# Optimization experiments

Hardware: AMD Instinct MI355X
Metric: run time of the kernel (lower is better)

## Reference

```python
import jax, jax.numpy as jnp
import numpy as np

NH = 16  # attention heads
TOPK = 50

def _rms(x, w):
    return x * jax.lax.rsqrt(jnp.mean(x * x, axis=-1, keepdims=True) + 1e-6) * w

def _rope(x, pos):
    # x: [1, T, NH, HD], pos: [T]
    half = x.shape[-1] // 2
    inv = 1.0 / (10000.0 ** (jnp.arange(half, dtype=jnp.float32) / half))
    ang = pos.astype(jnp.float32)[:, None] * inv[None, :]          # [T, half]
    cos = jnp.cos(ang)[None, :, None, :]
    sin = jnp.sin(ang)[None, :, None, :]
    x1, x2 = x[..., :half], x[..., half:]
    return jnp.concatenate([x1 * cos - x2 * sin, x2 * cos + x1 * sin], axis=-1)


def setup_inputs() -> dict:
    key = jax.random.key(0)
    ks = jax.random.split(key, 12)
    G, V, D, NL, FF = 15, 2048, 1024, 2, 4096
    s = 0.02
    return {
        'talker_hidden': jax.random.normal(ks[0], (1, 1, D), jnp.float32),
        'code_0_embed': jax.random.normal(ks[1], (1, 1, D), jnp.float32),
        'temperature': jnp.ones((1,), jnp.float32),
        'sample_uniforms': jax.random.uniform(ks[2], (G,), jnp.float32),
        'stacked_heads': jax.random.normal(ks[3], (G, V, D), jnp.float32) * s,
        'stacked_embeds': jax.random.normal(ks[4], (G, V, D), jnp.float32) * s,
        'ln1': jnp.ones((NL, D), jnp.float32),
        'ln2': jnp.ones((NL, D), jnp.float32),
        'ln_f': jnp.ones((D,), jnp.float32),
        'wq': jax.random.normal(ks[5], (NL, D, D), jnp.float32) * s,
        'wk': jax.random.normal(ks[6], (NL, D, D), jnp.float32) * s,
        'wv': jax.random.normal(ks[7], (NL, D, D), jnp.float32) * s,
        'wo': jax.random.normal(ks[8], (NL, D, D), jnp.float32) * s,
        'w1': jax.random.normal(ks[9], (NL, D, FF), jnp.float32) * s,
        'w2': jax.random.normal(ks[10], (NL, FF, D), jnp.float32) * s,
    }


def reference(talker_hidden, code_0_embed, temperature, sample_uniforms,
              stacked_heads, stacked_embeds, ln1, ln2, ln_f,
              wq, wk, wv, wo, w1, w2):
    NL = wq.shape[0]
    D = wq.shape[1]
    HD = D // NH
    G = stacked_heads.shape[0]

    def transformer_step(h, qpos, caches):
        # h: [1, T, D]; qpos: [T] absolute positions; caches: list of (k,v) or None
        new_caches = []
        for l in range(NL):
            T = h.shape[1]
            x = _rms(h, ln1[l])
            q = (x @ wq[l]).reshape(1, T, NH, HD)
            k = (x @ wk[l]).reshape(1, T, NH, HD)
            v = (x @ wv[l]).reshape(1, T, NH, HD)
            q = _rope(q, qpos)
            k = _rope(k, qpos)
            if caches is None:
                k_all, v_all = k, v
            else:
                k_all = jnp.concatenate([caches[l][0], k], axis=1)
                v_all = jnp.concatenate([caches[l][1], v], axis=1)
            new_caches.append((k_all, v_all))
            S = k_all.shape[1]
            scores = jnp.einsum('bthd,bshd->bhts', q, k_all) / jnp.sqrt(jnp.float32(HD))
            mask = jnp.arange(S)[None, :] <= qpos[:, None]      # [T, S] causal
            scores = jnp.where(mask[None, None], scores, jnp.float32(-1e30))
            attn = jax.nn.softmax(scores, axis=-1)
            out = jnp.einsum('bhts,bshd->bthd', attn, v_all).reshape(1, T, D)
            h = h + out @ wo[l]
            h = h + jax.nn.gelu((_rms(h, ln2[l])) @ w1[l]) @ w2[l]
        return _rms(h, ln_f), new_caches

    cp_input = jnp.concatenate([talker_hidden, code_0_embed], axis=1)  # [1, 2, D]
    h_seq, caches = transformer_step(cp_input, jnp.arange(2), None)
    hidden = h_seq[:, -1:, :]                                           # [1, 1, D]

    safe_temp = jnp.maximum(temperature.reshape(()), 1e-5)
    embed_sum = code_0_embed.reshape(-1)
    codes = []
    for g in range(G):
        logits = stacked_heads[g] @ hidden.reshape(-1)                  # [V]
        topv, topi = jax.lax.top_k(logits, TOPK)
        probs = jax.nn.softmax(topv / safe_temp)
        cdf = jnp.cumsum(probs)
        u = jnp.clip(sample_uniforms[g], 1e-6, 1.0 - 1e-6)
        choice = jnp.argmax((cdf >= u).astype(jnp.int32))
        code = topi[choice]
        codes.append(code.astype(jnp.int64))
        emb = stacked_embeds[g][code]                                   # [D]
        embed_sum = embed_sum + emb
        if g + 1 < G:
            h_seq, caches = transformer_step(emb[None, None, :],
                                             jnp.array([g + 2]), caches)
            hidden = h_seq[:, -1:, :]
    return jnp.stack(codes), embed_sum
```

## Files before the change

### kernel.cpp

```cpp
#include <hip/hip_runtime.h>
#include <math.h>

#define D      1024
#define NHEADS 16
#define HDIM   64
#define NL     2
#define FF     4096
#define NGRP   15
#define VOC    2048
#define TOPK   50
#define MAXS   16
#define NB     256
#define SLOT   16

struct Params {
    const float* talker; const float* code0; const float* temp; const float* unis;
    const float* heads;  const float* embeds;
    const float* ln1; const float* ln2; const float* lnf;
    const float* wq; const float* wk; const float* wv; const float* wo;
    const float* w1; const float* w2;
    float* out; float* ws;
};

__device__ __forceinline__ float cload(const float* p) {
    return __hip_atomic_load(p, __ATOMIC_RELAXED, __HIP_MEMORY_SCOPE_AGENT);
}
__device__ __forceinline__ void cstore(float* p, float v) {
    __hip_atomic_store(p, v, __ATOMIC_RELAXED, __HIP_MEMORY_SCOPE_AGENT);
}

__device__ __forceinline__ float wave_reduce_sum(float v) {
#pragma unroll
    for (int m = 32; m >= 1; m >>= 1) v += __shfl_xor(v, m, 64);
    return v;
}

__device__ __forceinline__ float geluf(float y) {
    return 0.5f * y * (1.f + tanhf(0.7978845608028654f * (y + 0.044715f * y * y * y)));
}

__device__ __forceinline__ void gsync(unsigned* arrive, unsigned* release, unsigned ep) {
    __syncthreads();
    const int bid = blockIdx.x, tid = threadIdx.x;
    if (tid == 0) {
        asm volatile("s_waitcnt vmcnt(0) lgkmcnt(0)" ::: "memory");
        __hip_atomic_store(&arrive[bid * SLOT], ep, __ATOMIC_RELAXED, __HIP_MEMORY_SCOPE_AGENT);
    }
    if (bid == 0) {
        while (__hip_atomic_load(&arrive[tid * SLOT], __ATOMIC_RELAXED,
                                 __HIP_MEMORY_SCOPE_AGENT) < ep)
            __builtin_amdgcn_s_sleep(4);
        __syncthreads();
        __hip_atomic_store(&release[tid * SLOT], ep, __ATOMIC_RELAXED, __HIP_MEMORY_SCOPE_AGENT);
    } else if (tid == 0) {
        while (__hip_atomic_load(&release[bid * SLOT], __ATOMIC_RELAXED,
                                 __HIP_MEMORY_SCOPE_AGENT) < ep)
            __builtin_amdgcn_s_sleep(4);
    }
    asm volatile("" ::: "memory");
    __syncthreads();
}

__device__ __forceinline__ void load_rms(const float* __restrict__ src,
                                         const float* __restrict__ w,
                                         float* xn, float* red) {
    int tid = threadIdx.x;
    float ss = 0.f;
    for (int i = tid; i < D; i += 256) { float v = cload(src + i); xn[i] = v; ss += v * v; }
    red[tid] = ss;
    __syncthreads();
    for (int s = 128; s > 0; s >>= 1) {
        if (tid < s) red[tid] += red[tid + s];
        __syncthreads();
    }
    float inv = rsqrtf(red[0] / (float)D + 1e-6f);
    for (int i = tid; i < D; i += 256) xn[i] = xn[i] * inv * w[i];
    __syncthreads();
}

__global__ __launch_bounds__(256) void k_pre(const float* __restrict__ th,
                                             const float* __restrict__ c0,
                                             float* __restrict__ h,
                                             float* __restrict__ out,
                                             float* __restrict__ qkv,
                                             unsigned* __restrict__ slots) {
    int i = blockIdx.x * 256 + threadIdx.x;
    if (i < 1024) {
        h[i] = th[i];
        h[D + i] = c0[i];
        out[NGRP + i] = c0[i];
    }
    for (int j = i; j < 2 * 3 * D; j += 2048) qkv[j] = 0.f;
    for (int j = i; j < 2 * NB * SLOT; j += 2048) slots[j] = 0u;
}

__global__ __launch_bounds__(256) void k_all(Params p) {
    __shared__ float xn[D];
    __shared__ float red[256];
    __shared__ float4 part[4][64];
    __shared__ float s_topv[TOPK];
    __shared__ int   s_topi[TOPK];
    __shared__ int   s_code;

    float* ws   = p.ws;
    float* h    = ws;
    float* qkvb = ws + 2048;
    float* ao   = ws + 8192;
    float* kc   = ws + 10240;
    float* vc   = ws + 43008;
    float* ub   = ws + 75776;
    float* lg   = ws + 83968;
    unsigned* arrive  = (unsigned*)(ws + 86016);
    unsigned* release = arrive + NB * SLOT;

    const int bid = blockIdx.x;
    const int tid = threadIdx.x;
    unsigned ep = 0;

    auto GS = [&]() { gsync(arrive, release, ++ep); };

    auto step = [&](int T, int basePos) {
        for (int l = 0; l < NL; ++l) {
            if (bid < 96 * T) {
                int x = bid % 12, y = (bid / 12) % 8, t = bid / 96;
                int m = x >> 2, ob = x & 3;
                load_rms(h + t * D, p.ln1 + l * D, xn, red);
                const float* W = ((m == 0) ? p.wq : (m == 1) ? p.wk : p.wv) + (long)l * D * D;
                int w = tid >> 6, lane = tid & 63;
                int obase = ob * 256;
                int kbase = (y * 4 + w) * 32;
                const float* Wp = W + (long)kbase * D + obase + lane * 4;
                float4 acc = {0.f, 0.f, 0.f, 0.f};
#pragma unroll 4
                for (int i = 0; i < 32; ++i) {
                    float xv = xn[kbase + i];
                    float4 wv4 = *(const float4*)(Wp + (long)i * D);
                    acc.x += xv * wv4.x; acc.y += xv * wv4.y;
                    acc.z += xv * wv4.z; acc.w += xv * wv4.w;
                }
                part[w][lane] = acc;
                __syncthreads();
                const float* pp = (const float*)part;
                float s = pp[tid] + pp[256 + tid] + pp[512 + tid] + pp[768 + tid];
                atomicAdd(&qkvb[t * 3 * D + m * D + obase + tid], s);
            }
            GS();

            {
                for (int i = bid * 256 + tid; i < T * FF; i += NB * 256) cstore(&ub[i], 0.f);
                int wid = bid * 4 + (tid >> 6);
                if (wid < T * NHEADS) {
                    int t = wid / NHEADS, hd = wid % NHEADS, d = tid & 63;
                    float* kcl = kc + (long)l * MAXS * D;
                    float* vcl = vc + (long)l * MAXS * D;
                    int pos = basePos + t;
                    int i = d & 31;
                    float inv = __expf(-(float)i * (9.210340371976184f / 32.0f));
                    float ang = (float)pos * inv;
                    float cs = cosf(ang), sn = sinf(ang);

                    float q = cload(&qkvb[t * 3 * D + hd * HDIM + d]);
                    float qp = __shfl_xor(q, 32, 64);
                    float qr = (d < 32) ? (q * cs - qp * sn) : (q * cs + qp * sn);

                    float k0 = cload(&qkvb[t * 3 * D + D + hd * HDIM + d]);
                    float kp = __shfl_xor(k0, 32, 64);
                    float kr = (d < 32) ? (k0 * cs - kp * sn) : (k0 * cs + kp * sn);

                    float v0 = cload(&qkvb[t * 3 * D + 2 * D + hd * HDIM + d]);
                    cstore(&kcl[pos * D + hd * HDIM + d], kr);
                    cstore(&vcl[pos * D + hd * HDIM + d], v0);

                    float sc[MAXS];
#pragma unroll
                    for (int s = 0; s < MAXS; ++s) {
                        if (s > pos) break;
                        float kv;
                        if (s < basePos) {
                            kv = cload(&kcl[s * D + hd * HDIM + d]);
                        } else if (s == pos) {
                            kv = kr;
                        } else {
                            float kk = cload(&qkvb[(s - basePos) * 3 * D + D + hd * HDIM + d]);
                            float kkp = __shfl_xor(kk, 32, 64);
                            float a2 = (float)s * inv;
                            float c2 = cosf(a2), s2 = sinf(a2);
                            kv = (d < 32) ? (kk * c2 - kkp * s2) : (kk * c2 + kkp * s2);
                        }
                        float dt = wave_reduce_sum(qr * kv);
                        sc[s] = dt * 0.125f;
                    }
                    float mx = -1e30f;
#pragma unroll
                    for (int s = 0; s < MAXS; ++s) { if (s > pos) break; mx = fmaxf(mx, sc[s]); }
                    float lsum = 0.f;
#pragma unroll
                    for (int s = 0; s < MAXS; ++s) { if (s > pos) break; sc[s] = expf(sc[s] - mx); lsum += sc[s]; }
                    float o = 0.f;
#pragma unroll
                    for (int s = 0; s < MAXS; ++s) {
                        if (s > pos) break;
                        float vv = (s < basePos) ? cload(&vcl[s * D + hd * HDIM + d])
                                                 : cload(&qkvb[(s - basePos) * 3 * D + 2 * D + hd * HDIM + d]);
                        o += sc[s] * vv;
                    }
                    cstore(&ao[t * D + hd * HDIM + d], o / lsum);
                }
            }
            GS();

            {
                for (int i = bid * 256 + tid; i < T * 3 * D; i += NB * 256) cstore(&qkvb[i], 0.f);
                if (bid < 64 * T) {
                    int x = bid % 4, y = (bid / 4) % 16, t = bid / 64;
                    const float* W = p.wo + (long)l * D * D;
                    for (int i = tid; i < D; i += 256) xn[i] = cload(&ao[t * D + i]);
                    __syncthreads();
                    int w = tid >> 6, lane = tid & 63;
                    int obase = x * 256;
                    int kbase = (y * 4 + w) * 16;
                    const float* Wp = W + (long)kbase * D + obase + lane * 4;
                    float4 acc = {0.f, 0.f, 0.f, 0.f};
#pragma unroll 4
                    for (int i = 0; i < 16; ++i) {
                        float xv = xn[kbase + i];
                        float4 wv4 = *(const float4*)(Wp + (long)i * D);
                        acc.x += xv * wv4.x; acc.y += xv * wv4.y;
                        acc.z += xv * wv4.z; acc.w += xv * wv4.w;
                    }
                    part[w][lane] = acc;
                    __syncthreads();
                    const float* pp = (const float*)part;
                    float s = pp[tid] + pp[256 + tid] + pp[512 + tid] + pp[768 + tid];
                    atomicAdd(&h[t * D + obase + tid], s);
                }
            }
            GS();

            if (bid < 128 * T) {
                int x = bid % 16, y = (bid / 16) % 8, t = bid / 128;
                load_rms(h + t * D, p.ln2 + l * D, xn, red);
                const float* W = p.w1 + (long)l * D * FF;
                int w = tid >> 6, lane = tid & 63;
                int obase = x * 256;
                int kbase = (y * 4 + w) * 32;
                const float* Wp = W + (long)kbase * FF + obase + lane * 4;
                float4 acc = {0.f, 0.f, 0.f, 0.f};
#pragma unroll 4
                for (int i = 0; i < 32; ++i) {
                    float xv = xn[kbase + i];
                    float4 wv4 = *(const float4*)(Wp + (long)i * FF);
                    acc.x += xv * wv4.x; acc.y += xv * wv4.y;
                    acc.z += xv * wv4.z; acc.w += xv * wv4.w;
                }
                part[w][lane] = acc;
                __syncthreads();
                const float* pp = (const float*)part;
                float s = pp[tid] + pp[256 + tid] + pp[512 + tid] + pp[768 + tid];
                atomicAdd(&ub[t * FF + obase + tid], s);
            }
            GS();

            if (bid < 128 * T) {
                int x = bid % 4, y = (bid / 4) % 32, t = bid / 128;
                int kblk = y * 128;
                if (tid < 128) red[tid] = geluf(cload(&ub[t * FF + kblk + tid]));
                __syncthreads();
                const float* W = p.w2 + (long)l * FF * D;
                int w = tid >> 6, lane = tid & 63;
                int obase = x * 256;
                int kloc = w * 32;
                const float* Wp = W + (long)(kblk + kloc) * D + obase + lane * 4;
                float4 acc = {0.f, 0.f, 0.f, 0.f};
#pragma unroll 4
                for (int i = 0; i < 32; ++i) {
                    float xv = red[kloc + i];
                    float4 wv4 = *(const float4*)(Wp + (long)i * D);
                    acc.x += xv * wv4.x; acc.y += xv * wv4.y;
                    acc.z += xv * wv4.z; acc.w += xv * wv4.w;
                }
                part[w][lane] = acc;
                __syncthreads();
                const float* pp = (const float*)part;
                float s = pp[tid] + pp[256 + tid] + pp[512 + tid] + pp[768 + tid];
                atomicAdd(&h[t * D + obase + tid], s);
            }
            GS();
        }
    };

    step(2, 0);

    for (int g = 0; g < NGRP; ++g) {
        {
            const float* hid = h + ((g == 0) ? D : 0);
            if (bid < 128) {
                load_rms(hid, p.lnf, xn, red);
                int lane = tid & 63, w = tid >> 6;
                int rbase = bid * 16 + w * 4;
                const float* Hd = p.heads + (long)g * VOC * D;
#pragma unroll
                for (int r = 0; r < 4; ++r) {
                    const float* row = Hd + (long)(rbase + r) * D;
                    float acc = 0.f;
#pragma unroll
                    for (int it = 0; it < 4; ++it) {
                        int idx = it * 256 + lane * 4;
                        float4 a = *(const float4*)(row + idx);
                        acc += a.x * xn[idx] + a.y * xn[idx + 1]
                             + a.z * xn[idx + 2] + a.w * xn[idx + 3];
                    }
                    acc = wave_reduce_sum(acc);
                    if (lane == 0) cstore(&lg[rbase + r], acc);
                }
            }
        }
        GS();

        if (bid == 0) {
            if (tid < 64) {
                int lane = tid;
                float v[32];
#pragma unroll
                for (int j = 0; j < 32; ++j) v[j] = cload(&lg[j * 64 + lane]);
                for (int r = 0; r < TOPK; ++r) {
                    float bv = v[0];
                    int bj = 0;
#pragma unroll
                    for (int j = 1; j < 32; ++j)
                        if (v[j] > bv) { bv = v[j]; bj = j; }
                    int bidx = bj * 64 + lane;
#pragma unroll
                    for (int m = 32; m >= 1; m >>= 1) {
                        float ov = __shfl_xor(bv, m, 64);
                        int oi = __shfl_xor(bidx, m, 64);
                        if (ov > bv || (ov == bv && oi < bidx)) { bv = ov; bidx = oi; }
                    }
                    if (lane == 0) { s_topv[r] = bv; s_topi[r] = bidx; }
                    if ((bidx & 63) == lane) v[bidx >> 6] = -3.0e38f;
                }
            }
            __syncthreads();
            if (tid == 0) {
                float t = fmaxf(p.temp[0], 1e-5f);
                float m = s_topv[0] / t;
                float pr[TOPK];
                float l = 0.f;
                for (int j = 0; j < TOPK; ++j) { pr[j] = expf(s_topv[j] / t - m); l += pr[j]; }
                float u = p.unis[g];
                u = fminf(fmaxf(u, 1e-6f), 1.f - 1e-6f);
                float cdf = 0.f;
                int choice = 0;
                bool found = false;
                for (int j = 0; j < TOPK; ++j) {
                    cdf += pr[j] / l;
                    if (!found && cdf >= u) { choice = j; found = true; }
                }
                s_code = s_topi[choice];
                p.out[g] = (float)s_code;
            }
            __syncthreads();
            int code = s_code;
            const float* e = p.embeds + ((long)g * VOC + code) * D;
            for (int i = tid; i < D; i += 256) {
                float ev = e[i];
                p.out[NGRP + i] += ev;
                cstore(&h[i], ev);
            }
        }
        GS();

        if (g + 1 < NGRP) step(1, g + 2);
    }
}

extern "C" void kernel_launch(void* const* d_in, const int* in_sizes, int n_in,
                              void* d_out, int out_size, void* d_ws, size_t ws_size,
                              hipStream_t stream) {
    const float* talker = (const float*)d_in[0];
    const float* code0  = (const float*)d_in[1];
    const float* temp   = (const float*)d_in[2];
    const float* unis   = (const float*)d_in[3];
    const float* heads  = (const float*)d_in[4];
    const float* embeds = (const float*)d_in[5];
    const float* ln1    = (const float*)d_in[6];
    const float* ln2    = (const float*)d_in[7];
    const float* lnf    = (const float*)d_in[8];
    const float* wq     = (const float*)d_in[9];
    const float* wk     = (const float*)d_in[10];
    const float* wv     = (const float*)d_in[11];
    const float* wo     = (const float*)d_in[12];
    const float* w1     = (const float*)d_in[13];
    const float* w2     = (const float*)d_in[14];
    float* out = (float*)d_out;

    float* ws   = (float*)d_ws;
    float* h    = ws;
    float* qkvb = ws + 2048;
    unsigned* slots = (unsigned*)(ws + 86016);

    k_pre<<<8, 256, 0, stream>>>(talker, code0, h, out, qkvb, slots);

    Params pr{talker, code0, temp, unis, heads, embeds, ln1, ln2, lnf,
              wq, wk, wv, wo, w1, w2, out, ws};
    k_all<<<dim3(NB), dim3(256), 0, stream>>>(pr);
}
```

Baseline: 2.391 ms.

## Prefetch weights into registers before grid barrier and split barrier into arrive/wait

Replaces the two-level arrive/release grid barrier with a single monotonic atomic counter, split into separate ARRIVE and WAITB phases. Each stage now issues its weight loads (QKV, WO, W1, W2, LM-head rows) into registers before waiting on the barrier, so the memory latency overlaps the synchronisation wait. Workspace zeroing and activation reads use 64-bit atomic accesses. This raises register pressure (launch bounds set to one block per SIMD) and puts all blocks on a single contended counter.

Result: slower. 3.178 ms (+32.9%).

```diff
diff --git a/kernel.cpp b/kernel.cpp
--- a/kernel.cpp
+++ b/kernel.cpp
@@ -11,7 +11,6 @@
 #define TOPK   50
 #define MAXS   16
 #define NB     256
-#define SLOT   16
 
 struct Params {
     const float* talker; const float* code0; const float* temp; const float* unis;
@@ -28,6 +27,14 @@
 __device__ __forceinline__ void cstore(float* p, float v) {
     __hip_atomic_store(p, v, __ATOMIC_RELAXED, __HIP_MEMORY_SCOPE_AGENT);
 }
+__device__ __forceinline__ unsigned long long cload64(const float* p) {
+    return __hip_atomic_load((const unsigned long long*)p, __ATOMIC_RELAXED,
+                             __HIP_MEMORY_SCOPE_AGENT);
+}
+__device__ __forceinline__ void cstore64(float* p, unsigned long long v) {
+    __hip_atomic_store((unsigned long long*)p, v, __ATOMIC_RELAXED,
+                       __HIP_MEMORY_SCOPE_AGENT);
+}
 
 __device__ __forceinline__ float wave_reduce_sum(float v) {
 #pragma unroll
@@ -37,28 +44,6 @@
 
 __device__ __forceinline__ float geluf(float y) {
     return 0.5f * y * (1.f + tanhf(0.7978845608028654f * (y + 0.044715f * y * y * y)));
-}
-
-__device__ __forceinline__ void gsync(unsigned* arrive, unsigned* release, unsigned ep) {
-    __syncthreads();
-    const int bid = blockIdx.x, tid = threadIdx.x;
-    if (tid == 0) {
-        asm volatile("s_waitcnt vmcnt(0) lgkmcnt(0)" ::: "memory");
-        __hip_atomic_store(&arrive[bid * SLOT], ep, __ATOMIC_RELAXED, __HIP_MEMORY_SCOPE_AGENT);
-    }
-    if (bid == 0) {
-        while (__hip_atomic_load(&arrive[tid * SLOT], __ATOMIC_RELAXED,
-                                 __HIP_MEMORY_SCOPE_AGENT) < ep)
-            __builtin_amdgcn_s_sleep(4);
-        __syncthreads();
-        __hip_atomic_store(&release[tid * SLOT], ep, __ATOMIC_RELAXED, __HIP_MEMORY_SCOPE_AGENT);
-    } else if (tid == 0) {
-        while (__hip_atomic_load(&release[bid * SLOT], __ATOMIC_RELAXED,
-                                 __HIP_MEMORY_SCOPE_AGENT) < ep)
-            __builtin_amdgcn_s_sleep(4);
-    }
-    asm volatile("" ::: "memory");
-    __syncthreads();
 }
 
 __device__ __forceinline__ void load_rms(const float* __restrict__ src,
@@ -83,18 +68,18 @@
                                              float* __restrict__ h,
                                              float* __restrict__ out,
                                              float* __restrict__ qkv,
-                                             unsigned* __restrict__ slots) {
+                                             unsigned* __restrict__ cnt) {
     int i = blockIdx.x * 256 + threadIdx.x;
+    if (i < 16) cnt[i] = 0u;
     if (i < 1024) {
         h[i] = th[i];
         h[D + i] = c0[i];
         out[NGRP + i] = c0[i];
     }
     for (int j = i; j < 2 * 3 * D; j += 2048) qkv[j] = 0.f;
-    for (int j = i; j < 2 * NB * SLOT; j += 2048) slots[j] = 0u;
-}
-
-__global__ __launch_bounds__(256) void k_all(Params p) {
+}
+
+__global__ __launch_bounds__(256, 1) void k_all(Params p) {
     __shared__ float xn[D];
     __shared__ float red[256];
     __shared__ float4 part[4][64];
@@ -110,44 +95,82 @@
     float* vc   = ws + 43008;
     float* ub   = ws + 75776;
     float* lg   = ws + 83968;
-    unsigned* arrive  = (unsigned*)(ws + 86016);
-    unsigned* release = arrive + NB * SLOT;
+    unsigned* cnt = (unsigned*)(ws + 86016);
 
     const int bid = blockIdx.x;
     const int tid = threadIdx.x;
     unsigned ep = 0;
 
-    auto GS = [&]() { gsync(arrive, release, ++ep); };
+    float4 rz[16];
+
+    auto ARRIVE = [&]() {
+        asm volatile("s_waitcnt vmcnt(0) lgkmcnt(0)" ::: "memory");
+        __syncthreads();
+        if (tid == 0)
+            __hip_atomic_fetch_add(cnt, 1u, __ATOMIC_RELAXED, __HIP_MEMORY_SCOPE_AGENT);
+    };
+    auto WAITB = [&]() {
+        ++ep;
+        unsigned tgt = ep * NB;
+        if (tid == 0) {
+            while (__hip_atomic_load(cnt, __ATOMIC_RELAXED, __HIP_MEMORY_SCOPE_AGENT) < tgt)
+                __builtin_amdgcn_s_sleep(8);
+        }
+        __syncthreads();
+    };
 
     auto step = [&](int T, int basePos) {
         for (int l = 0; l < NL; ++l) {
-            if (bid < 96 * T) {
+            {
+                bool act = bid < 96 * T;
+                float4 r[32];
                 int x = bid % 12, y = (bid / 12) % 8, t = bid / 96;
                 int m = x >> 2, ob = x & 3;
-                load_rms(h + t * D, p.ln1 + l * D, xn, red);
-                const float* W = ((m == 0) ? p.wq : (m == 1) ? p.wk : p.wv) + (long)l * D * D;
                 int w = tid >> 6, lane = tid & 63;
-                int obase = ob * 256;
-                int kbase = (y * 4 + w) * 32;
-                const float* Wp = W + (long)kbase * D + obase + lane * 4;
-                float4 acc = {0.f, 0.f, 0.f, 0.f};
-#pragma unroll 4
-                for (int i = 0; i < 32; ++i) {
-                    float xv = xn[kbase + i];
-                    float4 wv4 = *(const float4*)(Wp + (long)i * D);
-                    acc.x += xv * wv4.x; acc.y += xv * wv4.y;
-                    acc.z += xv * wv4.z; acc.w += xv * wv4.w;
-                }
-                part[w][lane] = acc;
-                __syncthreads();
-                const float* pp = (const float*)part;
-                float s = pp[tid] + pp[256 + tid] + pp[512 + tid] + pp[768 + tid];
-                atomicAdd(&qkvb[t * 3 * D + m * D + obase + tid], s);
-            }
-            GS();
+                int obase = ob * 256, kbase = (y * 4 + w) * 32;
+                if (act) {
+                    const float* W = ((m == 0) ? p.wq : (m == 1) ? p.wk : p.wv)
+                                     + (long)l * D * D;
+                    const float* Wp = W + (long)kbase * D + obase + lane * 4;
+#pragma unroll
+                    for (int i = 0; i < 32; ++i) r[i] = *(const float4*)(Wp + (long)i * D);
+                }
+                __builtin_amdgcn_sched_barrier(0);
+                WAITB();
+                if (act) {
+                    load_rms(h + t * D, p.ln1 + l * D, xn, red);
+                    float4 acc = {0.f, 0.f, 0.f, 0.f};
+#pragma unroll
+                    for (int i = 0; i < 32; ++i) {
+                        float xv = xn[kbase + i];
+                        acc.x += xv * r[i].x; acc.y += xv * r[i].y;
+                        acc.z += xv * r[i].z; acc.w += xv * r[i].w;
+                    }
+                    part[w][lane] = acc;
+                    __syncthreads();
+                    const float* pp2 = (const float*)part;
+                    float s = pp2[tid] + pp2[256 + tid] + pp2[512 + tid] + pp2[768 + tid];
+                    atomicAdd(&qkvb[t * 3 * D + m * D + obase + tid], s);
+                }
+                ARRIVE();
+            }
 
             {
-                for (int i = bid * 256 + tid; i < T * FF; i += NB * 256) cstore(&ub[i], 0.f);
+                bool wact = bid < 64 * T;
+                {
+                    int xw = bid % 4, yw = (bid / 4) % 16;
+                    int w = tid >> 6, lane = tid & 63;
+                    if (wact) {
+                        const float* WpO = p.wo + (long)l * D * D
+                                         + (long)((yw * 4 + w) * 16) * D + xw * 256 + lane * 4;
+#pragma unroll
+                        for (int i = 0; i < 16; ++i) rz[i] = *(const float4*)(WpO + (long)i * D);
+                    }
+                }
+                __builtin_amdgcn_sched_barrier(0);
+                WAITB();
+                for (int i = bid * 256 + tid; i < T * (FF / 2); i += NB * 256)
+                    cstore64(&ub[2 * i], 0ull);
                 int wid = bid * 4 + (tid >> 6);
                 if (wid < T * NHEADS) {
                     int t = wid / NHEADS, hd = wid % NHEADS, d = tid & 63;
@@ -195,180 +218,222 @@
                     for (int s = 0; s < MAXS; ++s) { if (s > pos) break; mx = fmaxf(mx, sc[s]); }
                     float lsum = 0.f;
 #pragma unroll
-                    for (int s = 0; s < MAXS; ++s) { if (s > pos) break; sc[s] = expf(sc[s] - mx); lsum += sc[s]; }
-                    float o = 0.f;
-#pragma unroll
                     for (int s = 0; s < MAXS; ++s) {
                         if (s > pos) break;
-                        float vv = (s < basePos) ? cload(&vcl[s * D + hd * HDIM + d])
-                                                 : cload(&qkvb[(s - basePos) * 3 * D + 2 * D + hd * HDIM + d]);
+                        sc[s] = expf(sc[s] - mx); lsum += sc[s];
+                    }
+                    float o = 0.f;
+#pragma unroll
+                    for (int s = 0; s < MAXS; ++s) {
+                        if (s > pos) break;
+                        float vv = (s < basePos)
+                                 ? cload(&vcl[s * D + hd * HDIM + d])
+                                 : cload(&qkvb[(s - basePos) * 3 * D + 2 * D + hd * HDIM + d]);
                         o += sc[s] * vv;
                     }
                     cstore(&ao[t * D + hd * HDIM + d], o / lsum);
                 }
-            }
-            GS();
+                ARRIVE();
+            }
 
             {
-                for (int i = bid * 256 + tid; i < T * 3 * D; i += NB * 256) cstore(&qkvb[i], 0.f);
+                WAITB();
+                for (int i = bid * 256 + tid; i < T * 3 * (D / 2); i += NB * 256)
+                    cstore64(&qkvb[2 * i], 0ull);
                 if (bid < 64 * T) {
                     int x = bid % 4, y = (bid / 4) % 16, t = bid / 64;
-                    const float* W = p.wo + (long)l * D * D;
-                    for (int i = tid; i < D; i += 256) xn[i] = cload(&ao[t * D + i]);
+                    for (int jj = tid; jj < D / 2; jj += 256) {
+                        unsigned long long u = cload64(ao + t * D + 2 * jj);
+                        xn[2 * jj]     = __uint_as_float((unsigned)u);
+                        xn[2 * jj + 1] = __uint_as_float((unsigned)(u >> 32));
+                    }
                     __syncthreads();
                     int w = tid >> 6, lane = tid & 63;
-                    int obase = x * 256;
-                    int kbase = (y * 4 + w) * 16;
-                    const float* Wp = W + (long)kbase * D + obase + lane * 4;
+                    int obase = x * 256, kbase = (y * 4 + w) * 16;
                     float4 acc = {0.f, 0.f, 0.f, 0.f};
-#pragma unroll 4
+#pragma unroll
                     for (int i = 0; i < 16; ++i) {
                         float xv = xn[kbase + i];
-                        float4 wv4 = *(const float4*)(Wp + (long)i * D);
-                        acc.x += xv * wv4.x; acc.y += xv * wv4.y;
-                        acc.z += xv * wv4.z; acc.w += xv * wv4.w;
+                        acc.x += xv * rz[i].x; acc.y += xv * rz[i].y;
+                        acc.z += xv * rz[i].z; acc.w += xv * rz[i].w;
                     }
                     part[w][lane] = acc;
                     __syncthreads();
-                    const float* pp = (const float*)part;
-                    float s = pp[tid] + pp[256 + tid] + pp[512 + tid] + pp[768 + tid];
+                    const float* pp2 = (const float*)part;
+                    float s = pp2[tid] + pp2[256 + tid] + pp2[512 + tid] + pp2[768 + tid];
                     atomicAdd(&h[t * D + obase + tid], s);
                 }
-            }
-            GS();
-
-            if (bid < 128 * T) {
+                ARRIVE();
+            }
+
+            {
+                bool act = bid < 128 * T;
+                float4 r[32];
                 int x = bid % 16, y = (bid / 16) % 8, t = bid / 128;
-                load_rms(h + t * D, p.ln2 + l * D, xn, red);
-                const float* W = p.w1 + (long)l * D * FF;
                 int w = tid >> 6, lane = tid & 63;
-                int obase = x * 256;
-                int kbase = (y * 4 + w) * 32;
-                const float* Wp = W + (long)kbase * FF + obase + lane * 4;
-                float4 acc = {0.f, 0.f, 0.f, 0.f};
-#pragma unroll 4
-                for (int i = 0; i < 32; ++i) {
-                    float xv = xn[kbase + i];
-                    float4 wv4 = *(const float4*)(Wp + (long)i * FF);
-                    acc.x += xv * wv4.x; acc.y += xv * wv4.y;
-                    acc.z += xv * wv4.z; acc.w += xv * wv4.w;
-                }
-                part[w][lane] = acc;
-                __syncthreads();
-                const float* pp = (const float*)part;
-                float s = pp[tid] + pp[256 + tid] + pp[512 + tid] + pp[768 + tid];
-                atomicAdd(&ub[t * FF + obase + tid], s);
-            }
-            GS();
-
-            if (bid < 128 * T) {
+                int obase = x * 256, kbase = (y * 4 + w) * 32;
+                if (act) {
+                    const float* Wp = p.w1 + (long)l * D * FF + (long)kbase * FF
+                                    + obase + lane * 4;
+#pragma unroll
+                    for (int i = 0; i < 32; ++i) r[i] = *(const float4*)(Wp + (long)i * FF);
+                }
+                __builtin_amdgcn_sched_barrier(0);
+                WAITB();
+                if (act) {
+                    load_rms(h + t * D, p.ln2 + l * D, xn, red);
+                    float4 acc = {0.f, 0.f, 0.f, 0.f};
+#pragma unroll
+                    for (int i = 0; i < 32; ++i) {
+                        float xv = xn[kbase + i];
+                        acc.x += xv * r[i].x; acc.y += xv * r[i].y;
+                        acc.z += xv * r[i].z; acc.w += xv * r[i].w;
+                    }
+                    part[w][lane] = acc;
+                    __syncthreads();
+                    const float* pp2 = (const float*)part;
+                    float s = pp2[tid] + pp2[256 + tid] + pp2[512 + tid] + pp2[768 + tid];
+                    atomicAdd(&ub[t * FF + obase + tid], s);
+                }
+                ARRIVE();
+            }
+
+            {
+                bool act = bid < 128 * T;
+                float4 r[32];
                 int x = bid % 4, y = (bid / 4) % 32, t = bid / 128;
                 int kblk = y * 128;
-                if (tid < 128) red[tid] = geluf(cload(&ub[t * FF + kblk + tid]));
-                __syncthreads();
-                const float* W = p.w2 + (long)l * FF * D;
                 int w = tid >> 6, lane = tid & 63;
-                int obase = x * 256;
-                int kloc = w * 32;
-                const float* Wp = W + (long)(kblk + kloc) * D + obase + lane * 4;
-                float4 acc = {0.f, 0.f, 0.f, 0.f};
-#pragma unroll 4
-                for (int i = 0; i < 32; ++i) {
-                    float xv = red[kloc + i];
-                    float4 wv4 = *(const float4*)(Wp + (long)i * D);
-                    acc.x += xv * wv4.x; acc.y += xv * wv4.y;
-                    acc.z += xv * wv4.z; acc.w += xv * wv4.w;
-                }
-                part[w][lane] = acc;
-                __syncthreads();
-                const float* pp = (const float*)part;
-                float s = pp[tid] + pp[256 + tid] + pp[512 + tid] + pp[768 + tid];
-                atomicAdd(&h[t * D + obase + tid], s);
-            }
-            GS();
+                int obase = x * 256, kloc = w * 32;
+                if (act) {
+                    const float* Wp = p.w2 + (long)l * FF * D + (long)(kblk + kloc) * D
+                                    + obase + lane * 4;
+#pragma unroll
+                    for (int i = 0; i < 32; ++i) r[i] = *(const float4*)(Wp + (long)i * D);
+                }
+                __builtin_amdgcn_sched_barrier(0);
+                WAITB();
+                if (act) {
+                    if (tid < 64) {
+                        unsigned long long u = cload64(&ub[t * FF + kblk + 2 * tid]);
+                        red[2 * tid]     = geluf(__uint_as_float((unsigned)u));
+                        red[2 * tid + 1] = geluf(__uint_as_float((unsigned)(u >> 32)));
+                    }
+                    __syncthreads();
+                    float4 acc = {0.f, 0.f, 0.f, 0.f};
+#pragma unroll
+                    for (int i = 0; i < 32; ++i) {
+                        float xv = red[kloc + i];
+                        acc.x += xv * r[i].x; acc.y += xv * r[i].y;
+                        acc.z += xv * r[i].z; acc.w += xv * r[i].w;
+                    }
+                    part[w][lane] = acc;
+                    __syncthreads();
+                    const float* pp2 = (const float*)part;
+                    float s = pp2[tid] + pp2[256 + tid] + pp2[512 + tid] + pp2[768 + tid];
+                    atomicAdd(&h[t * D + obase + tid], s);
+                }
+                ARRIVE();
+            }
         }
     };
 
+    ARRIVE();
     step(2, 0);
 
     for (int g = 0; g < NGRP; ++g) {
         {
-            const float* hid = h + ((g == 0) ? D : 0);
-            if (bid < 128) {
+            bool act = bid < 128;
+            float4 r[16];
+            int lane = tid & 63, w = tid >> 6;
+            int rbase = bid * 16 + w * 4;
+            if (act) {
+                const float* Hd = p.heads + (long)g * VOC * D;
+#pragma unroll
+                for (int rr = 0; rr < 4; ++rr) {
+                    const float* row = Hd + (long)(rbase + rr) * D;
+#pragma unroll
+                    for (int it = 0; it < 4; ++it)
+                        r[rr * 4 + it] = *(const float4*)(row + it * 256 + lane * 4);
+                }
+            }
+            __builtin_amdgcn_sched_barrier(0);
+            WAITB();
+            if (act) {
+                const float* hid = h + ((g == 0) ? D : 0);
                 load_rms(hid, p.lnf, xn, red);
-                int lane = tid & 63, w = tid >> 6;
-                int rbase = bid * 16 + w * 4;
-                const float* Hd = p.heads + (long)g * VOC * D;
-#pragma unroll
-                for (int r = 0; r < 4; ++r) {
-                    const float* row = Hd + (long)(rbase + r) * D;
+#pragma unroll
+                for (int rr = 0; rr < 4; ++rr) {
                     float acc = 0.f;
 #pragma unroll
                     for (int it = 0; it < 4; ++it) {
                         int idx = it * 256 + lane * 4;
-                        float4 a = *(const float4*)(row + idx);
+                        float4 a = r[rr * 4 + it];
                         acc += a.x * xn[idx] + a.y * xn[idx + 1]
                              + a.z * xn[idx + 2] + a.w * xn[idx + 3];
                     }
                     acc = wave_reduce_sum(acc);
-                    if (lane == 0) cstore(&lg[rbase + r], acc);
-                }
-            }
+                    if (lane == 0) cstore(&lg[rbase + rr], acc);
+                }
+            }
+            ARRIVE();
         }
-        GS();
-
-        if (bid == 0) {
-            if (tid < 64) {
-                int lane = tid;
-                float v[32];
-#pragma unroll
-                for (int j = 0; j < 32; ++j) v[j] = cload(&lg[j * 64 + lane]);
-                for (int r = 0; r < TOPK; ++r) {
-                    float bv = v[0];
-                    int bj = 0;
-#pragma unroll
-                    for (int j = 1; j < 32; ++j)
-                        if (v[j] > bv) { bv = v[j]; bj = j; }
-                    int bidx = bj * 64 + lane;
-#pragma unroll
-                    for (int m = 32; m >= 1; m >>= 1) {
-                        float ov = __shfl_xor(bv, m, 64);
-                        int oi = __shfl_xor(bidx, m, 64);
-                        if (ov > bv || (ov == bv && oi < bidx)) { bv = ov; bidx = oi; }
-                    }
-                    if (lane == 0) { s_topv[r] = bv; s_topi[r] = bidx; }
-                    if ((bidx & 63) == lane) v[bidx >> 6] = -3.0e38f;
-                }
-            }
-            __syncthreads();
-            if (tid == 0) {
-                float t = fmaxf(p.temp[0], 1e-5f);
-                float m = s_topv[0] / t;
-                float pr[TOPK];
-                float l = 0.f;
-                for (int j = 0; j < TOPK; ++j) { pr[j] = expf(s_topv[j] / t - m); l += pr[j]; }
-                float u = p.unis[g];
-                u = fminf(fmaxf(u, 1e-6f), 1.f - 1e-6f);
-                float cdf = 0.f;
-                int choice = 0;
-                bool found = false;
-                for (int j = 0; j < TOPK; ++j) {
-                    cdf += pr[j] / l;
-                    if (!found && cdf >= u) { choice = j; found = true; }
-                }
-                s_code = s_topi[choice];
-                p.out[g] = (float)s_code;
-            }
-            __syncthreads();
-            int code = s_code;
-            const float* e = p.embeds + ((long)g * VOC + code) * D;
-            for (int i = tid; i < D; i += 256) {
-                float ev = e[i];
-                p.out[NGRP + i] += ev;
-                cstore(&h[i], ev);
-            }
+
+        {
+            WAITB();
+            if (bid == 0) {
+                if (tid < 64) {
+                    int lane = tid;
+                    float v[32];
+#pragma unroll
+                    for (int j = 0; j < 32; ++j) v[j] = cload(&lg[j * 64 + lane]);
+                    for (int r = 0; r < TOPK; ++r) {
+                        float bv = v[0];
+                        int bj = 0;
+#pragma unroll
+                        for (int j = 1; j < 32; ++j)
+                            if (v[j] > bv) { bv = v[j]; bj = j; }
+                        int bidx = bj * 64 + lane;
+#pragma unroll
+                        for (int m = 32; m >= 1; m >>= 1) {
+                            float ov = __shfl_xor(bv, m, 64);
+                            int oi = __shfl_xor(bidx, m, 64);
+                            if (ov > bv || (ov == bv && oi < bidx)) { bv = ov; bidx = oi; }
+                        }
+                        if (lane == 0) { s_topv[r] = bv; s_topi[r] = bidx; }
+                        if ((bidx & 63) == lane) v[bidx >> 6] = -3.0e38f;
+                    }
+                }
+                __syncthreads();
+                if (tid == 0) {
+                    float t = fmaxf(p.temp[0], 1e-5f);
+                    float m = s_topv[0] / t;
+                    float pr[TOPK];
+                    float l = 0.f;
+                    for (int j = 0; j < TOPK; ++j) { pr[j] = expf(s_topv[j] / t - m); l += pr[j]; }
+                    float u = p.unis[g];
+                    u = fminf(fmaxf(u, 1e-6f), 1.f - 1e-6f);
+                    float cdf = 0.f;
+                    int choice = 0;
+                    bool found = false;
+                    for (int j = 0; j < TOPK; ++j) {
+                        cdf += pr[j] / l;
+                        if (!found && cdf >= u) { choice = j; found = true; }
+                    }
+                    s_code = s_topi[choice];
+                    p.out[g] = (float)s_code;
+                }
+                __syncthreads();
+                int code = s_code;
+                const float* e = p.embeds + ((long)g * VOC + code) * D;
+                for (int i = tid; i < D; i += 256) {
+                    float ev = e[i];
+                    p.out[NGRP + i] += ev;
+                    cstore(&h[i], ev);
+                }
+            }
+            ARRIVE();
         }
-        GS();
 
         if (g + 1 < NGRP) step(1, g + 2);
     }
@@ -397,9 +462,9 @@
     float* ws   = (float*)d_ws;
     float* h    = ws;
     float* qkvb = ws + 2048;
-    unsigned* slots = (unsigned*)(ws + 86016);
-
-    k_pre<<<8, 256, 0, stream>>>(talker, code0, h, out, qkvb, slots);
+    unsigned* cnt = (unsigned*)(ws + 86016);
+
+    k_pre<<<8, 256, 0, stream>>>(talker, code0, h, out, qkvb, cnt);
 
     Params pr{talker, code0, temp, unis, heads, embeds, ln1, ln2, lnf,
               wq, wk, wv, wo, w1, w2, out, ws};
```
